# Kernel tuning notes

Measured on AMD Instinct MI355X. Metric: run time of the kernel, lower is better.

The kernel has to match this reference:

```python
import jax, jax.numpy as jnp
import numpy as np

H = 8          # num_heads (in_channels > 8)
BN_EPS = 1e-5  # torch BatchNorm2d default


def _l2norm(w):
    # torch.norm(w, 2, dim=-2, keepdim=True) + 1e-4
    return jnp.sqrt(jnp.sum(w * w, axis=-2, keepdims=True)) + 1e-4


def setup_inputs() -> dict:
    key = jax.random.key(0)
    ks = jax.random.split(key, 6)
    N, C, T, V = 64, 128, 128, 25
    x = jax.random.normal(ks[0], (N, C, T, V), dtype=jnp.float32)
    fc1 = jax.random.normal(ks[1], (3, H, V, V), dtype=jnp.float32)
    rpe = jax.random.normal(ks[2], (3, H, V), dtype=jnp.float32)
    hops = jax.random.randint(ks[3], (V, V), 0, V)
    fc2_w = jax.random.normal(ks[4], (3, C, C // H), dtype=jnp.float32) * 0.1
    fc2_b = jax.random.normal(ks[5], (3, C), dtype=jnp.float32) * 0.1
    gamma = jnp.ones((C,), dtype=jnp.float32)
    beta = jnp.zeros((C,), dtype=jnp.float32)
    return {"x": x, "fc1": fc1, "rpe": rpe, "hops": hops,
            "fc2_w": fc2_w, "fc2_b": fc2_b, "gamma": gamma, "beta": beta}


def reference(x, fc1, rpe, hops, fc2_w, fc2_b, gamma, beta):
    N, C, T, V = x.shape
    c = C // H
    # relative-position embedding gathered by hop distance: (3, H, V, V)
    pos_emb = rpe[:, :, hops]
    x_in = x.reshape(N, H, c, T, V)
    y = jnp.zeros((N, H, c, T, V), dtype=x.dtype)
    for i in range(3):
        # normalized adaptive adjacency + normalized positional term
        w1 = fc1[i] / _l2norm(fc1[i]) + pos_emb[i] / _l2norm(pos_emb[i])  # (H, V, V)
        z = jnp.einsum('nhctv,hvw->nhctw', x_in, w1)
        # grouped 1x1 conv == per-head channel mixing
        wg = fc2_w[i].reshape(H, c, c)                       # (H, out_per_group, in_per_group)
        z = jnp.einsum('nhctv,hdc->nhdtv', z, wg)
        z = z + fc2_b[i].reshape(1, H, c, 1, 1)
        y = y + z
    y = y.reshape(N, C, T, V)
    # BatchNorm2d (training-mode batch statistics, biased variance)
    mean = jnp.mean(y, axis=(0, 2, 3), keepdims=True)
    var = jnp.var(y, axis=(0, 2, 3), keepdims=True)
    y = gamma.reshape(1, C, 1, 1) * (y - mean) * jax.lax.rsqrt(var + BN_EPS) + beta.reshape(1, C, 1, 1)
    # residual (in_channels == out_channels -> identity down) + ReLU
    return jax.nn.relu(y + x)
```

## Files before the change

kernel.cpp:

```cpp
#include <hip/hip_runtime.h>
#include <hip/hip_bf16.h>

namespace {

constexpr int kN = 64, kC = 128, kT = 128, kV = 25, kH = 8, kc = 16;
constexpr int kKS = 13;
constexpr int kBCol = 448;
constexpr int kBStep = kBCol * 32;
constexpr int kXRow = 416;

typedef __attribute__((ext_vector_type(8))) short bf16x8;
typedef __attribute__((ext_vector_type(8))) unsigned short u16x8;
typedef __attribute__((ext_vector_type(4))) float f32x4;

__device__ inline unsigned short f2bf(float f) {
    unsigned int u = __builtin_bit_cast(unsigned int, f);
    u += 0x7fffu + ((u >> 16) & 1u);
    return (unsigned short)(u >> 16);
}
__device__ inline float bf2f(unsigned short s) {
    return __builtin_bit_cast(float, ((unsigned int)s) << 16);
}
__device__ inline void glds16(const void* g, void* l) {
    __builtin_amdgcn_global_load_lds(
        (const __attribute__((address_space(1))) void*)g,
        (__attribute__((address_space(3))) void*)l, 16, 0, 0);
}

__global__ void precompute_w1(const float* __restrict__ fc1,
                              const float* __restrict__ rpe,
                              const int* __restrict__ hops,
                              float* __restrict__ W1) {
    int ih = blockIdx.x;
    int w = threadIdx.x;
    if (w >= kV) return;
    const float* f = fc1 + ih * kV * kV;
    const float* r = rpe + ih * kV;
    float s1 = 0.f, s2 = 0.f;
    for (int v = 0; v < kV; ++v) {
        float a = f[v * kV + w];
        float p = r[hops[v * kV + w]];
        s1 += a * a; s2 += p * p;
    }
    float n1 = sqrtf(s1) + 1e-4f, n2 = sqrtf(s2) + 1e-4f;
    float* o = W1 + ih * kV * kV;
    for (int v = 0; v < kV; ++v) {
        float a = f[v * kV + w];
        float p = r[hops[v * kV + w]];
        o[v * kV + w] = a / n1 + p / n2;
    }
}

__global__ void precompute_W(const float* __restrict__ W1,
                             const float* __restrict__ fc2_w,
                             unsigned short* __restrict__ Wt3) {
    int k = blockIdx.x;
    int h = blockIdx.y;
    unsigned short* outp = Wt3 + ((size_t)h * kKS + k) * kBStep;
    for (int e = threadIdx.x; e < kBStep; e += 256) {
        int col = e >> 5, lo = e & 31;
        int kap = k * 32 + lo;
        int c = kap / 26, vv = kap - c * 26;
        float val = 0.f;
        if (vv < 25 && col < 400) {
            int d = col / 25, w = col - d * 25;
            #pragma unroll
            for (int i = 0; i < 3; ++i) {
                float wg = fc2_w[(i * kC + h * kc + d) * kc + c];
                float w1 = W1[((i * kH + h) * kV + vv) * kV + w];
                val += wg * w1;
            }
        }
        outp[e] = f2bf(val);
    }
}

__global__ __launch_bounds__(256, 2) void gemm_y(const float* __restrict__ x,
                                                 const unsigned short* __restrict__ Wt3,
                                                 unsigned short* __restrict__ yb,
                                                 float2* __restrict__ Pbuf) {
    __shared__ __align__(16) unsigned short XY[64 * kXRow];
    __shared__ __align__(16) float bounce[6400];

    const int tb = blockIdx.x, n = blockIdx.y, h = blockIdx.z;
    const int tid = threadIdx.x, lane = tid & 63, wv = tid >> 6;
    const int ll = lane & 15, lh = lane >> 4;
    const int t0 = tb * 64;

    const float* xbase = x + ((size_t)(n * kC + h * kc) * kT + t0) * kV;
    const unsigned short* bbase = Wt3 + (size_t)h * kKS * kBStep
                                + ((size_t)(wv * 7) * 16 + ll) * 32 + lh * 8;

    for (int s = 0; s < 4; ++s) {
        #pragma unroll
        for (int q = 0; q < 7; ++q) {
            int e = q * 256 + tid;
            if (e < 1600) {
                int c = e / 400, off = e - c * 400;
                glds16(xbase + (size_t)(s * 4 + c) * 3200 + off * 4,
                       (char*)bounce + (size_t)e * 16);
            }
        }
        __syncthreads();
        {
            const int t = lane, t13 = t % 13;
            const float* bp = bounce + wv * 1600 + t * 25;
            unsigned int* xw = (unsigned int*)&XY[0] + t * (kXRow / 2) + (s * 4 + wv) * 13;
            #pragma unroll
            for (int i = 0; i < 13; ++i) {
                int p = i + t13; if (p >= 13) p -= 13;
                float f0 = bp[2 * p];
                float f1 = (p < 12) ? bp[2 * p + 1] : 0.f;
                xw[p] = (unsigned)f2bf(f0) | ((unsigned)f2bf(f1) << 16);
            }
        }
        __syncthreads();
    }

    f32x4 acc[4][7];
    #pragma unroll
    for (int a = 0; a < 4; ++a)
        #pragma unroll
        for (int b = 0; b < 7; ++b) acc[a][b] = (f32x4)(0.f);

    auto bld = [&](int k, int ci) -> bf16x8 {
        return *(const bf16x8*)(bbase + (size_t)k * kBStep + ci * 512);
    };
    auto amfma = [&](int k, const bf16x8 (&bf)[7]) {
        bf16x8 a0 = *(const bf16x8*)&XY[(size_t)(0 * 16 + ll) * kXRow + k * 32 + lh * 8];
        bf16x8 a1 = *(const bf16x8*)&XY[(size_t)(1 * 16 + ll) * kXRow + k * 32 + lh * 8];
        bf16x8 a2 = *(const bf16x8*)&XY[(size_t)(2 * 16 + ll) * kXRow + k * 32 + lh * 8];
        bf16x8 a3 = *(const bf16x8*)&XY[(size_t)(3 * 16 + ll) * kXRow + k * 32 + lh * 8];
        #pragma unroll
        for (int ci = 0; ci < 7; ++ci) {
            acc[0][ci] = __builtin_amdgcn_mfma_f32_16x16x32_bf16(a0, bf[ci], acc[0][ci], 0, 0, 0);
            acc[1][ci] = __builtin_amdgcn_mfma_f32_16x16x32_bf16(a1, bf[ci], acc[1][ci], 0, 0, 0);
            acc[2][ci] = __builtin_amdgcn_mfma_f32_16x16x32_bf16(a2, bf[ci], acc[2][ci], 0, 0, 0);
            acc[3][ci] = __builtin_amdgcn_mfma_f32_16x16x32_bf16(a3, bf[ci], acc[3][ci], 0, 0, 0);
        }
    };

    bf16x8 bA[7], bB[7];
    #pragma unroll
    for (int ci = 0; ci < 7; ++ci) bA[ci] = bld(0, ci);

    int k = 0;
    #pragma unroll 1
    for (int it = 0; it < 6; ++it, k += 2) {
        #pragma unroll
        for (int ci = 0; ci < 7; ++ci) bB[ci] = bld(k + 1, ci);
        amfma(k, bA);
        #pragma unroll
        for (int ci = 0; ci < 7; ++ci) bA[ci] = bld(k + 2, ci);
        amfma(k + 1, bB);
    }
    amfma(12, bA);

    __syncthreads();
    #pragma unroll
    for (int rf = 0; rf < 4; ++rf) {
        #pragma unroll
        for (int r = 0; r < 4; ++r) {
            int t = rf * 16 + lh * 4 + r;
            #pragma unroll
            for (int ci = 0; ci < 7; ++ci) {
                int m = wv * 112 + ci * 16 + ll;
                if (m < 400) {
                    int d = m / 25, w = m - d * 25;
                    XY[d * 1600 + t * 25 + w] = f2bf(acc[rf][ci][r]);
                }
            }
        }
    }

    float2* Bs = (float2*)&bounce[0];
    #pragma unroll
    for (int ci = 0; ci < 7; ++ci) {
        float s = 0.f, ss = 0.f;
        #pragma unroll
        for (int rf = 0; rf < 4; ++rf)
            #pragma unroll
            for (int r = 0; r < 4; ++r) {
                float v = acc[rf][ci][r];
                s += v; ss += v * v;
            }
        s  += __shfl_xor(s, 16);  ss += __shfl_xor(ss, 16);
        s  += __shfl_xor(s, 32);  ss += __shfl_xor(ss, 32);
        if (lh == 0) Bs[wv * 112 + ci * 16 + ll] = make_float2(s, ss);
    }
    __syncthreads();

    unsigned short* ybase = yb + ((size_t)(n * kC + h * kc) * kT + t0) * kV;
    #pragma unroll
    for (int q = 0; q < 13; ++q) {
        int e = q * 256 + tid;
        if (e < 3200) {
            int d = e / 200, c = e - d * 200;
            u16x8 valv = *(const u16x8*)&XY[d * 1600 + c * 8];
            *(u16x8*)(ybase + (size_t)d * (kT * kV) + c * 8) = valv;
        }
    }

    if (tid < 16) {
        float s = 0.f, ss = 0.f;
        for (int w = 0; w < 25; ++w) {
            float2 p = Bs[tid * 25 + w];
            s += p.x; ss += p.y;
        }
        size_t bid = (size_t)tb + 2 * ((size_t)n + 64 * (size_t)h);
        Pbuf[bid * 16 + tid] = make_float2(s, ss);
    }
}

__global__ void bn_finalize(const float2* __restrict__ Pbuf,
                            const float* __restrict__ gamma,
                            const float* __restrict__ beta,
                            float2* __restrict__ scsh) {
    int ch = threadIdx.x;
    if (ch >= kC) return;
    int h = ch >> 4, d = ch & 15;
    float s = 0.f, ss = 0.f;
    for (int j = 0; j < 128; ++j) {
        float2 p = Pbuf[(size_t)(j + 128 * h) * 16 + d];
        s += p.x; ss += p.y;
    }
    const float inv = 1.f / (float)(kN * kT * kV);
    float mean = s * inv;
    float var  = ss * inv - mean * mean;
    float sc = gamma[ch] * rsqrtf(var + 1e-5f);
    scsh[ch] = make_float2(sc, beta[ch] - mean * sc);
}

__global__ void bn_apply(const unsigned short* __restrict__ yb,
                         const float* __restrict__ x,
                         const float2* __restrict__ scsh,
                         float* __restrict__ out) {
    const size_t total8 = (size_t)kN * kC * kT * kV / 8;
    for (size_t i = (size_t)blockIdx.x * blockDim.x + threadIdx.x; i < total8;
         i += (size_t)gridDim.x * blockDim.x) {
        int ch = (int)((i / 400) % kC);
        float2 sc = scsh[ch];
        u16x8 yv = ((const u16x8*)yb)[i];
        f32x4 x0 = ((const f32x4*)x)[i * 2];
        f32x4 x1 = ((const f32x4*)x)[i * 2 + 1];
        f32x4 o0, o1;
        #pragma unroll
        for (int q = 0; q < 4; ++q) {
            o0[q] = fmaxf(bf2f((unsigned short)yv[q]) * sc.x + sc.y + x0[q], 0.f);
            o1[q] = fmaxf(bf2f((unsigned short)yv[q + 4]) * sc.x + sc.y + x1[q], 0.f);
        }
        ((f32x4*)out)[i * 2]     = o0;
        ((f32x4*)out)[i * 2 + 1] = o1;
    }
}

}

extern "C" void kernel_launch(void* const* d_in, const int* in_sizes, int n_in,
                              void* d_out, int out_size, void* d_ws, size_t ws_size,
                              hipStream_t stream) {
    const float* x     = (const float*)d_in[0];
    const float* fc1   = (const float*)d_in[1];
    const float* rpe   = (const float*)d_in[2];
    const int*   hops  = (const int*)d_in[3];
    const float* fc2w  = (const float*)d_in[4];
    const float* gamma = (const float*)d_in[6];
    const float* beta  = (const float*)d_in[7];
    float* out = (float*)d_out;

    char* ws = (char*)d_ws;
    unsigned short* yb   = (unsigned short*)ws;
    float*          W1   = (float*)(ws + 52428800);
    unsigned short* Wt3  = (unsigned short*)(ws + 52494336);
    float2*         Pbuf = (float2*)(ws + 55476224);
    float2*         scsh = (float2*)(ws + 55607296);

    precompute_w1<<<24, 32, 0, stream>>>(fc1, rpe, hops, W1);
    precompute_W<<<dim3(13, 8), 256, 0, stream>>>(W1, fc2w, Wt3);
    gemm_y<<<dim3(2, 64, 8), 256, 0, stream>>>(x, Wt3, yb, Pbuf);
    bn_finalize<<<1, 128, 0, stream>>>(Pbuf, gamma, beta, scsh);
    bn_apply<<<2048, 256, 0, stream>>>(yb, x, scsh, out);
}
```

Measured before the change: 135.3 us.

## Merge two time-tiles into one 512-thread block sharing weight loads

The gemm_y kernel now processes the full T=128 range per (n,h) with 512 threads arranged as 2 row groups by 4 column groups, instead of two 64-row blocks of 256 threads. The two row groups read the same weight columns, so more data is shared within a block, and the x loads and yb stores become contiguous spans per channel slice. The partial-stat buffer and bn_finalize are shrunk to match. In exchange, LDS per block doubles to about 157KB, occupancy drops to one block per CU, and the grid is halved to 512 blocks.

```diff
diff --git a/kernel.cpp b/kernel.cpp
--- a/kernel.cpp
+++ b/kernel.cpp
@@ -75,37 +75,35 @@
     }
 }
 
-__global__ __launch_bounds__(256, 2) void gemm_y(const float* __restrict__ x,
+__global__ __launch_bounds__(512, 1) void gemm_y(const float* __restrict__ x,
                                                  const unsigned short* __restrict__ Wt3,
                                                  unsigned short* __restrict__ yb,
                                                  float2* __restrict__ Pbuf) {
-    __shared__ __align__(16) unsigned short XY[64 * kXRow];
-    __shared__ __align__(16) float bounce[6400];
-
-    const int tb = blockIdx.x, n = blockIdx.y, h = blockIdx.z;
+    __shared__ __align__(16) unsigned short XY[128 * kXRow];
+    __shared__ __align__(16) float bounce[12800];
+
+    const int h = blockIdx.x, n = blockIdx.y;
     const int tid = threadIdx.x, lane = tid & 63, wv = tid >> 6;
+    const int rg = wv >> 2, cg = wv & 3;
     const int ll = lane & 15, lh = lane >> 4;
-    const int t0 = tb * 64;
-
-    const float* xbase = x + ((size_t)(n * kC + h * kc) * kT + t0) * kV;
+
+    const float* xbase = x + (size_t)(n * kC + h * kc) * (kT * kV);
     const unsigned short* bbase = Wt3 + (size_t)h * kKS * kBStep
-                                + ((size_t)(wv * 7) * 16 + ll) * 32 + lh * 8;
+                                + ((size_t)(cg * 112) + ll) * 32 + lh * 8;
 
     for (int s = 0; s < 4; ++s) {
         #pragma unroll
         for (int q = 0; q < 7; ++q) {
-            int e = q * 256 + tid;
-            if (e < 1600) {
-                int c = e / 400, off = e - c * 400;
-                glds16(xbase + (size_t)(s * 4 + c) * 3200 + off * 4,
+            int e = q * 512 + tid;
+            if (e < 3200)
+                glds16(xbase + (size_t)s * 12800 + (size_t)e * 4,
                        (char*)bounce + (size_t)e * 16);
-            }
         }
         __syncthreads();
         {
-            const int t = lane, t13 = t % 13;
-            const float* bp = bounce + wv * 1600 + t * 25;
-            unsigned int* xw = (unsigned int*)&XY[0] + t * (kXRow / 2) + (s * 4 + wv) * 13;
+            const int c = tid & 3, t = tid >> 2, t13 = t % 13;
+            const float* bp = bounce + c * 3200 + t * 25;
+            unsigned int* xw = (unsigned int*)&XY[0] + t * (kXRow / 2) + (s * 4 + c) * 13;
             #pragma unroll
             for (int i = 0; i < 13; ++i) {
                 int p = i + t13; if (p >= 13) p -= 13;
@@ -127,10 +125,10 @@
         return *(const bf16x8*)(bbase + (size_t)k * kBStep + ci * 512);
     };
     auto amfma = [&](int k, const bf16x8 (&bf)[7]) {
-        bf16x8 a0 = *(const bf16x8*)&XY[(size_t)(0 * 16 + ll) * kXRow + k * 32 + lh * 8];
-        bf16x8 a1 = *(const bf16x8*)&XY[(size_t)(1 * 16 + ll) * kXRow + k * 32 + lh * 8];
-        bf16x8 a2 = *(const bf16x8*)&XY[(size_t)(2 * 16 + ll) * kXRow + k * 32 + lh * 8];
-        bf16x8 a3 = *(const bf16x8*)&XY[(size_t)(3 * 16 + ll) * kXRow + k * 32 + lh * 8];
+        bf16x8 a0 = *(const bf16x8*)&XY[(size_t)(rg * 64 + 0 * 16 + ll) * kXRow + k * 32 + lh * 8];
+        bf16x8 a1 = *(const bf16x8*)&XY[(size_t)(rg * 64 + 1 * 16 + ll) * kXRow + k * 32 + lh * 8];
+        bf16x8 a2 = *(const bf16x8*)&XY[(size_t)(rg * 64 + 2 * 16 + ll) * kXRow + k * 32 + lh * 8];
+        bf16x8 a3 = *(const bf16x8*)&XY[(size_t)(rg * 64 + 3 * 16 + ll) * kXRow + k * 32 + lh * 8];
         #pragma unroll
         for (int ci = 0; ci < 7; ++ci) {
             acc[0][ci] = __builtin_amdgcn_mfma_f32_16x16x32_bf16(a0, bf[ci], acc[0][ci], 0, 0, 0);
@@ -161,13 +159,13 @@
     for (int rf = 0; rf < 4; ++rf) {
         #pragma unroll
         for (int r = 0; r < 4; ++r) {
-            int t = rf * 16 + lh * 4 + r;
+            int t = rg * 64 + rf * 16 + lh * 4 + r;
             #pragma unroll
             for (int ci = 0; ci < 7; ++ci) {
-                int m = wv * 112 + ci * 16 + ll;
+                int m = cg * 112 + ci * 16 + ll;
                 if (m < 400) {
                     int d = m / 25, w = m - d * 25;
-                    XY[d * 1600 + t * 25 + w] = f2bf(acc[rf][ci][r]);
+                    XY[d * 3200 + t * 25 + w] = f2bf(acc[rf][ci][r]);
                 }
             }
         }
@@ -186,29 +184,26 @@
             }
         s  += __shfl_xor(s, 16);  ss += __shfl_xor(ss, 16);
         s  += __shfl_xor(s, 32);  ss += __shfl_xor(ss, 32);
-        if (lh == 0) Bs[wv * 112 + ci * 16 + ll] = make_float2(s, ss);
+        if (lh == 0) Bs[rg * 448 + cg * 112 + ci * 16 + ll] = make_float2(s, ss);
     }
     __syncthreads();
 
-    unsigned short* ybase = yb + ((size_t)(n * kC + h * kc) * kT + t0) * kV;
+    unsigned short* ybase = yb + (size_t)(n * kC + h * kc) * (kT * kV);
     #pragma unroll
     for (int q = 0; q < 13; ++q) {
-        int e = q * 256 + tid;
-        if (e < 3200) {
-            int d = e / 200, c = e - d * 200;
-            u16x8 valv = *(const u16x8*)&XY[d * 1600 + c * 8];
-            *(u16x8*)(ybase + (size_t)d * (kT * kV) + c * 8) = valv;
-        }
+        int e = q * 512 + tid;
+        if (e < 6400)
+            *(u16x8*)(ybase + (size_t)e * 8) = *(const u16x8*)&XY[(size_t)e * 8];
     }
 
     if (tid < 16) {
         float s = 0.f, ss = 0.f;
         for (int w = 0; w < 25; ++w) {
-            float2 p = Bs[tid * 25 + w];
-            s += p.x; ss += p.y;
-        }
-        size_t bid = (size_t)tb + 2 * ((size_t)n + 64 * (size_t)h);
-        Pbuf[bid * 16 + tid] = make_float2(s, ss);
+            float2 p0 = Bs[tid * 25 + w];
+            float2 p1 = Bs[448 + tid * 25 + w];
+            s += p0.x + p1.x; ss += p0.y + p1.y;
+        }
+        Pbuf[((size_t)n + 64 * (size_t)h) * 16 + tid] = make_float2(s, ss);
     }
 }
 
@@ -220,8 +215,8 @@
     if (ch >= kC) return;
     int h = ch >> 4, d = ch & 15;
     float s = 0.f, ss = 0.f;
-    for (int j = 0; j < 128; ++j) {
-        float2 p = Pbuf[(size_t)(j + 128 * h) * 16 + d];
+    for (int j = 0; j < 64; ++j) {
+        float2 p = Pbuf[(size_t)(j + 64 * h) * 16 + d];
         s += p.x; ss += p.y;
     }
     const float inv = 1.f / (float)(kN * kT * kV);
@@ -277,7 +272,7 @@
 
     precompute_w1<<<24, 32, 0, stream>>>(fc1, rpe, hops, W1);
     precompute_W<<<dim3(13, 8), 256, 0, stream>>>(W1, fc2w, Wt3);
-    gemm_y<<<dim3(2, 64, 8), 256, 0, stream>>>(x, Wt3, yb, Pbuf);
+    gemm_y<<<dim3(8, 64), 512, 0, stream>>>(x, Wt3, yb, Pbuf);
     bn_finalize<<<1, 128, 0, stream>>>(Pbuf, gamma, beta, scsh);
     bn_apply<<<2048, 256, 0, stream>>>(yb, x, scsh, out);
 }
```

After: 134.6 us. No clear change (-0.5%).
